# Optimization experiments

Hardware: AMD Instinct MI355X
Metric: run time of the kernel (lower is better)

## Reference

```python
import jax, jax.numpy as jnp
import numpy as np
import math

NUM_HEADS = 16
HEAD_DIM = 64
NUM_BUCKETS = 256
MAX_DISTANCE = 16384
ROPE_BASE = 10000.0


def _rel_pos_bucket(rel):
    # faithful to RelativePositionEncoding._relative_position_bucket
    ab = jnp.abs(rel)
    max_exact = NUM_BUCKETS // 4  # 64
    half = NUM_BUCKETS // 2       # 128
    is_small = ab < max_exact
    safe = jnp.maximum(ab, 1).astype(jnp.float32)
    large = max_exact + (jnp.log(safe / max_exact) / math.log(MAX_DISTANCE / max_exact) * (half - max_exact)).astype(jnp.int32)
    large = jnp.minimum(large, half - 1)
    bucket = jnp.where(is_small, ab, large)
    bucket = jnp.where(rel < 0, half + bucket, bucket)
    return bucket


def _rope_cos_sin(seq_len):
    # RotaryPositionEncoding with rope dim = 2*head_dim: num_features = head_dim,
    # inv_freq over arange(0, head_dim, 2)/head_dim, interleaved repeat to head_dim
    inv_freq = 1.0 / (ROPE_BASE ** (jnp.arange(0, HEAD_DIM, 2, dtype=jnp.float32) / HEAD_DIM))
    pos = jnp.arange(seq_len, dtype=jnp.float32)
    freqs = pos[:, None] * inv_freq[None, :]          # [S, HEAD_DIM//2]
    cos = jnp.repeat(jnp.cos(freqs), 2, axis=-1)      # [S, HEAD_DIM]
    sin = jnp.repeat(jnp.sin(freqs), 2, axis=-1)
    return cos, sin


def _rotate_half(t):
    h = t.shape[-1] // 2
    return jnp.concatenate([-t[..., h:], t[..., :h]], axis=-1)


def setup_inputs() -> dict:
    key = jax.random.key(0)
    ks = jax.random.split(key, 6)
    B, S, E = 2, 2048, 1024
    x = jax.random.normal(ks[0], (B, S, E), dtype=jnp.float32)
    Wq = jax.random.normal(ks[1], (E, E), dtype=jnp.float32) * 0.02
    Wk = jax.random.normal(ks[2], (E, E), dtype=jnp.float32) * 0.02
    Wv = jax.random.normal(ks[3], (E, E), dtype=jnp.float32) * 0.02
    Wo = jax.random.normal(ks[4], (E, E), dtype=jnp.float32) * 0.02
    rel_emb = jax.random.normal(ks[5], (NUM_BUCKETS, NUM_HEADS, HEAD_DIM), dtype=jnp.float32) * 0.02
    return {"x": x, "Wq": Wq, "Wk": Wk, "Wv": Wv, "Wo": Wo, "rel_emb": rel_emb}


def reference(x, Wq, Wk, Wv, Wo, rel_emb):
    B, S, E = x.shape
    H, D = NUM_HEADS, HEAD_DIM

    def split_heads(t):
        return t.reshape(B, S, H, D).transpose(0, 2, 1, 3)  # [B,H,S,D]

    q = split_heads(x @ Wq)
    k = split_heads(x @ Wk)
    v = split_heads(x @ Wv)

    # inline RoPE on q/k (cos/sin broadcast over batch & heads)
    cos, sin = _rope_cos_sin(S)  # [S, D]
    q = q * cos + _rotate_half(q) * sin
    k = k * cos + _rotate_half(k) * sin

    # relative-position bucket bias: q . rel_emb[bucket(i-j)]
    pos = jnp.arange(S)
    bucket = _rel_pos_bucket(pos[:, None] - pos[None, :])      # [S, S]
    q_rel = jnp.einsum('bhqd,nhd->bhqn', q, rel_emb)           # [B,H,S,NUM_BUCKETS]
    bias = jnp.take_along_axis(q_rel, bucket[None, None, :, :], axis=-1)  # [B,H,S,S]

    scale = 1.0 / math.sqrt(D)
    scores = (jnp.einsum('bhqd,bhkd->bhqk', q, k) + bias) * scale

    causal = pos[:, None] >= pos[None, :]
    scores = jnp.where(causal[None, None], scores, jnp.float32(-1e9))
    attn = jax.nn.softmax(scores, axis=-1)

    out = jnp.einsum('bhqk,bhkd->bhqd', attn, v)
    out = out.transpose(0, 2, 1, 3).reshape(B, S, E)
    return out @ Wo
```

## Files before the change

kernel.cpp:

```cpp
#include <hip/hip_runtime.h>
#include <hip/hip_bf16.h>
#include <math.h>


typedef __attribute__((ext_vector_type(8))) short bf16x8;
typedef __attribute__((ext_vector_type(4))) float f32x4;

static __device__ __forceinline__ unsigned short f2bf(float x) {
    unsigned u = __float_as_uint(x);
    unsigned r = (u + 0x7fffu + ((u >> 16) & 1u)) >> 16;
    return (unsigned short)r;
}
static __device__ __forceinline__ float bf2f(unsigned short h) {
    return __uint_as_float(((unsigned)h) << 16);
}
static __device__ __forceinline__ unsigned cvtpk(float lo, float hi) {
    unsigned r;
    asm("v_cvt_pk_bf16_f32 %0, %1, %2" : "=v"(r) : "v"(lo), "v"(hi));
    return r;
}
static __device__ __forceinline__ float fexp2(float x) {
    return __builtin_amdgcn_exp2f(x);
}

#define GLOAD16(gp, lp)                                                            \
    __builtin_amdgcn_global_load_lds(                                              \
        (const __attribute__((address_space(1))) unsigned int*)(gp),               \
        (__attribute__((address_space(3))) unsigned int*)(lp), 16, 0, 0)

__global__ void prep(const float* __restrict__ x,
                     const float* __restrict__ W0, const float* __restrict__ W1,
                     const float* __restrict__ W2, const float* __restrict__ W3,
                     const float* __restrict__ rel,
                     unsigned short* __restrict__ xb,
                     unsigned short* __restrict__ T0, unsigned short* __restrict__ T1,
                     unsigned short* __restrict__ T2, unsigned short* __restrict__ T3,
                     unsigned short* __restrict__ relTb)
{
    __shared__ unsigned short tls[64][65];
    const int id  = blockIdx.x;
    const int tid = threadIdx.x;
    if (id < 2048) {
        const size_t t = (size_t)id * 256 + tid;
        const float4* p = (const float4*)(x + t*8);
        float4 a = p[0], b = p[1];
        unsigned w0 = cvtpk(a.x, a.y), w1 = cvtpk(a.z, a.w);
        unsigned w2 = cvtpk(b.x, b.y), w3 = cvtpk(b.z, b.w);
        *(uint4*)(xb + t*8) = make_uint4(w0, w1, w2, w3);
    } else if (id < 3072) {
        const int local = id - 2048;
        const int z  = local >> 8;
        const float* W = (z == 0) ? W0 : (z == 1) ? W1 : (z == 2) ? W2 : W3;
        unsigned short* Wt = (z == 0) ? T0 : (z == 1) ? T1 : (z == 2) ? T2 : T3;
        const int bb  = local & 255;
        const int bxt = bb & 15;
        const int byt = bb >> 4;
        const int r   = tid >> 2;
        const int c0  = (tid & 3) * 16;
        const float* src = W + (size_t)(byt*64 + r)*1024 + bxt*64 + c0;
#pragma unroll
        for (int j = 0; j < 4; ++j) {
            float4 vv = ((const float4*)src)[j];
            tls[c0 + j*4 + 0][r] = f2bf(vv.x);
            tls[c0 + j*4 + 1][r] = f2bf(vv.y);
            tls[c0 + j*4 + 2][r] = f2bf(vv.z);
            tls[c0 + j*4 + 3][r] = f2bf(vv.w);
        }
        __syncthreads();
        unsigned short* dst = Wt + (size_t)(bxt*64 + r)*1024 + byt*64 + c0;
        unsigned w[8];
#pragma unroll
        for (int j = 0; j < 8; ++j)
            w[j] = (unsigned)tls[r][c0 + 2*j] | ((unsigned)tls[r][c0 + 2*j + 1] << 16);
        *(uint4*)(dst)     = make_uint4(w[0], w[1], w[2], w[3]);
        *(uint4*)(dst + 8) = make_uint4(w[4], w[5], w[6], w[7]);
    } else {
        const int t  = (id - 3072) * 256 + tid;
        const int d0 = (t & 7) * 8;
        const int n  = (t >> 3) & 127;
        const int h  = t >> 10;
        const float* src = rel + ((size_t)(n*16 + h))*64 + d0;
        float4 a = ((const float4*)src)[0], b = ((const float4*)src)[1];
        unsigned w0 = cvtpk(a.x, a.y), w1 = cvtpk(a.z, a.w);
        unsigned w2 = cvtpk(b.x, b.y), w3 = cvtpk(b.z, b.w);
        *(uint4*)(relTb + (size_t)h*8192 + n*64 + d0) = make_uint4(w0, w1, w2, w3);
    }
}

#define GEMM_STAGE(t, buf)                                                             \
    {                                                                                  \
        const int k0s = (t) * 64;                                                      \
        _Pragma("unroll")                                                              \
        for (int j = 0; j < 4; ++j) {                                                  \
            GLOAD16(agp + (size_t)(j*32 + srow)*1024 + k0s, &Als[buf][0] + j*2048 + tid*8); \
            GLOAD16(bgp + (size_t)(j*32 + srow)*1024 + k0s, &Bls[buf][0] + j*2048 + tid*8); \
        }                                                                              \
    }

#define GEMM_COMPUTE(buf)                                                              \
    {                                                                                  \
        _Pragma("unroll")                                                              \
        for (int ks = 0; ks < 2; ++ks) {                                               \
            bf16x8 af[4], bfr[4];                                                      \
            _Pragma("unroll")                                                          \
            for (int m = 0; m < 4; ++m)                                                \
                af[m] = *(const bf16x8*)&Als[buf][(wr + m*16 + (lane & 15))*64 + ks*32 + (lane >> 4)*8]; \
            _Pragma("unroll")                                                          \
            for (int n = 0; n < 4; ++n)                                                \
                bfr[n] = *(const bf16x8*)&Bls[buf][(wc + n*16 + (lane & 15))*64 + ks*32 + (lane >> 4)*8]; \
            _Pragma("unroll")                                                          \
            for (int m = 0; m < 4; ++m)                                                \
                _Pragma("unroll")                                                      \
                for (int n = 0; n < 4; ++n)                                            \
                    acc[m][n] = __builtin_amdgcn_mfma_f32_16x16x32_bf16(af[m], bfr[n], acc[m][n], 0, 0, 0); \
        }                                                                              \
    }

__global__ __launch_bounds__(256) void gemm_qkv(const unsigned short* __restrict__ A,
    const unsigned short* __restrict__ wtq, const unsigned short* __restrict__ wtk,
    const unsigned short* __restrict__ wtv,
    unsigned short* __restrict__ qb, unsigned short* __restrict__ kbb,
    unsigned short* __restrict__ vTb)
{
    __shared__ __align__(16) unsigned short Als[2][8192];
    __shared__ __align__(16) unsigned short Bls[2][8192];
    const int z = blockIdx.z;
    const unsigned short* Bt = (z == 0) ? wtq : (z == 1) ? wtk : wtv;

    const int tid  = threadIdx.x;
    const int wave = tid >> 6, lane = tid & 63;
    const int wr = (wave >> 1) * 64, wc = (wave & 1) * 64;
    const int bx = blockIdx.x, by = blockIdx.y;
    const int srow = tid >> 3;
    const unsigned short* agp = A  + (size_t)(by*128)*1024 + (tid & 7)*8;
    const unsigned short* bgp = Bt + (size_t)(bx*128)*1024 + (tid & 7)*8;

    f32x4 acc[4][4];
#pragma unroll
    for (int m = 0; m < 4; ++m)
#pragma unroll
        for (int n = 0; n < 4; ++n) acc[m][n] = (f32x4)0.f;

    GEMM_STAGE(0, 0);
    __syncthreads();
    int cur = 0;
    for (int t = 0; t < 16; ++t) {
        if (t < 15) GEMM_STAGE(t + 1, cur ^ 1);
        GEMM_COMPUTE(cur);
        __syncthreads();
        cur ^= 1;
    }

    if (z == 2) {
#pragma unroll
        for (int m = 0; m < 4; ++m) {
            const int r0 = by*128 + wr + m*16 + (lane >> 4)*4;
#pragma unroll
            for (int n = 0; n < 4; ++n) {
                const int col = bx*128 + wc + n*16 + (lane & 15);
                const int bb = r0 >> 11, ss = r0 & 2047;
                const int hh = col >> 6, dd = col & 63;
                unsigned r01 = cvtpk(acc[m][n][0], acc[m][n][1]);
                unsigned r23 = cvtpk(acc[m][n][2], acc[m][n][3]);
                *(uint2*)(vTb + (((size_t)bb*16 + hh)*64 + dd)*2048 + ss) = make_uint2(r01, r23);
            }
        }
    } else {
        unsigned short* O = z ? kbb : qb;
        const float CC = 0.41524101186092029f;
        const float qscl = z ? 1.0f : 0.1803368801111204f;
#pragma unroll
        for (int n = 0; n < 2; ++n) {
            const int dd = n*16 + (lane & 15);
            const float if0 = exp2f(-(float)(dd >> 1) * CC);
            const float if1 = exp2f(-(float)(16 + (dd >> 1)) * CC);
            const int col = bx*128 + wc + n*16 + (lane & 15);
            const int hh = col >> 6;
#pragma unroll
            for (int m = 0; m < 4; ++m) {
                const int r0 = by*128 + wr + m*16 + (lane >> 4)*4;
#pragma unroll
                for (int rg = 0; rg < 4; ++rg) {
                    const int row = r0 + rg;
                    const int bb = row >> 11, s = row & 2047;
                    const float x0 = acc[m][n][rg];
                    const float x1 = acc[m][n + 2][rg];
                    const float a0 = (float)s * if0;
                    const float a1 = (float)s * if1;
                    const float o0 = (x0 * __cosf(a0) - x1 * __sinf(a0)) * qscl;
                    const float o1 = (x1 * __cosf(a1) + x0 * __sinf(a1)) * qscl;
                    unsigned short* ob = O + (((size_t)bb*16 + hh)*2048 + s)*64 + dd;
                    ob[0]  = f2bf(o0);
                    ob[32] = f2bf(o1);
                }
            }
        }
    }
}

__global__ __launch_bounds__(256) void gemm_o(const unsigned short* __restrict__ A,
                                              const unsigned short* __restrict__ Bt,
                                              float* __restrict__ C)
{
    __shared__ __align__(16) unsigned short Als[2][8192];
    __shared__ __align__(16) unsigned short Bls[2][8192];
    const int tid  = threadIdx.x;
    const int wave = tid >> 6, lane = tid & 63;
    const int wr = (wave >> 1) * 64, wc = (wave & 1) * 64;
    const int bx = blockIdx.x, by = blockIdx.y;
    const int srow = tid >> 3;
    const unsigned short* agp = A  + (size_t)(by*128)*1024 + (tid & 7)*8;
    const unsigned short* bgp = Bt + (size_t)(bx*128)*1024 + (tid & 7)*8;

    f32x4 acc[4][4];
#pragma unroll
    for (int m = 0; m < 4; ++m)
#pragma unroll
        for (int n = 0; n < 4; ++n) acc[m][n] = (f32x4)0.f;

    GEMM_STAGE(0, 0);
    __syncthreads();
    int cur = 0;
    for (int t = 0; t < 16; ++t) {
        if (t < 15) GEMM_STAGE(t + 1, cur ^ 1);
        GEMM_COMPUTE(cur);
        __syncthreads();
        cur ^= 1;
    }

#pragma unroll
    for (int m = 0; m < 4; ++m) {
        const int r0 = by*128 + wr + m*16 + (lane >> 4)*4;
#pragma unroll
        for (int n = 0; n < 4; ++n) {
            const int col = bx*128 + wc + n*16 + (lane & 15);
#pragma unroll
            for (int rg = 0; rg < 4; ++rg)
                C[(size_t)(r0 + rg)*1024 + col] = acc[m][n][rg];
        }
    }
}

__global__ __launch_bounds__(256) void qrel_mfma(const unsigned short* __restrict__ qb,
                                                 const unsigned short* __restrict__ relTb,
                                                 unsigned short* __restrict__ qrelb)
{
    __shared__ __align__(16) unsigned short Rls[8192];
    __shared__ __align__(16) unsigned short Qls[8192];
    const int tid  = threadIdx.x;
    const int wave = tid >> 6, lane = tid & 63;
    const int wr = (wave >> 1) * 64;
    const int wc = (wave & 1) * 64;
    const int s0 = blockIdx.x * 128;
    const int bh = blockIdx.y;
    const int h  = bh & 15;

    const unsigned short* qsrc = qb + ((size_t)bh*2048 + s0)*64;
    const unsigned short* rsrc = relTb + (size_t)h*8192;
#pragma unroll
    for (int j = 0; j < 4; ++j) {
        GLOAD16(rsrc + j*2048 + tid*8, &Rls[0] + j*2048 + tid*8);
        GLOAD16(qsrc + j*2048 + tid*8, &Qls[0] + j*2048 + tid*8);
    }

    f32x4 acc[4][4];
#pragma unroll
    for (int m = 0; m < 4; ++m)
#pragma unroll
        for (int n = 0; n < 4; ++n) acc[m][n] = (f32x4)0.f;

    __syncthreads();

#pragma unroll
    for (int ks = 0; ks < 2; ++ks) {
        bf16x8 rf[4], qf[4];
#pragma unroll
        for (int m = 0; m < 4; ++m)
            rf[m] = *(const bf16x8*)&Rls[(wr + m*16 + (lane & 15))*64 + ks*32 + (lane >> 4)*8];
#pragma unroll
        for (int n = 0; n < 4; ++n)
            qf[n] = *(const bf16x8*)&Qls[(wc + n*16 + (lane & 15))*64 + ks*32 + (lane >> 4)*8];
#pragma unroll
        for (int m = 0; m < 4; ++m)
#pragma unroll
            for (int n = 0; n < 4; ++n)
                acc[m][n] = __builtin_amdgcn_mfma_f32_16x16x32_bf16(rf[m], qf[n], acc[m][n], 0, 0, 0);
    }

#pragma unroll
    for (int m = 0; m < 4; ++m) {
        const int bkt0 = wr + m*16 + (lane >> 4)*4;
#pragma unroll
        for (int n = 0; n < 4; ++n) {
            const int srow = s0 + wc + n*16 + (lane & 15);
            unsigned r01 = cvtpk(acc[m][n][0], acc[m][n][1]);
            unsigned r23 = cvtpk(acc[m][n][2], acc[m][n][3]);
            *(uint2*)(qrelb + ((size_t)bh*2048 + srow)*128 + bkt0) = make_uint2(r01, r23);
        }
    }
}

__global__ __launch_bounds__(256) void flash_mfma(
    const unsigned short* __restrict__ qb, const unsigned short* __restrict__ kb,
    const unsigned short* __restrict__ vT, const unsigned short* __restrict__ qrelb,
    unsigned short* __restrict__ ctxb)
{
    __shared__ __align__(16) unsigned short kls[2][4096];
    __shared__ __align__(16) unsigned short vtls[2][4096];
    __shared__ __align__(16) unsigned short qrels[64*136];
    __shared__ unsigned short btbl[2048];

    const int tid = threadIdx.x;
    const int id  = blockIdx.x;
    const int bh  = id & 31;
    const int px  = id >> 5;

    const int w   = tid >> 6;
    const int l   = tid & 63;
    const int q15 = l & 15;
    const int g   = l >> 4;

    for (int idx = tid; idx < 2048; idx += 256) {
        int bkt;
        if (idx < 64) bkt = idx;
        else {
            bkt = 64 + (int)(__log2f((float)idx) * 8.0f - 48.0f);
            bkt = bkt > 127 ? 127 : bkt;
        }
        btbl[idx] = (unsigned short)(bkt * 2);
    }

    const size_t headoff = (size_t)bh * 2048 * 64;
    const unsigned short* gbase;
    int jstride;
    if (tid < 128) { gbase = kb + headoff; jstride = 64; }
    else           { gbase = vT + headoff; jstride = 1;  }
    int soff[4], doff[4];
#pragma unroll
    for (int i = 0; i < 4; ++i) {
        const int D = (tid & 127)*16 + i*2048;
        const int r = D >> 7, c = (D >> 4) & 7;
        soff[i] = (tid < 128) ? (r*64 + ((c ^ (r & 7))*8))
                              : (r*2048 + ((c ^ (r & 7))*8));
        doff[i] = D;
    }

    const char* qrow_base = (const char*)qrels + (w*16 + q15) * 272;
    const int srcA = ((2*g) & 3)*16 + q15;
    const int srcB = ((2*g + 1) & 3)*16 + q15;

    int cur = 0;
    for (int pp = 0; pp < 2; ++pp) {
        const int bxc = pp ? (31 - px) : px;
        const int i0  = bxc * 64;
        const int iq  = i0 + w*16 + q15;

        __syncthreads();
        for (int idx = tid; idx < 1024; idx += 256) {
            const int r = idx >> 4, c8 = idx & 15;
            uint4 vv = *(const uint4*)(qrelb + ((size_t)bh*2048 + i0 + r)*128 + c8*8);
            *(uint4*)&qrels[r*136 + c8*8] = vv;
        }
        {
            char* lb = (tid < 128) ? (char*)kls[cur] : (char*)vtls[cur];
#pragma unroll
            for (int i = 0; i < 4; ++i) GLOAD16(gbase + soff[i], lb + doff[i]);
        }

        bf16x8 qf0, qf1;
        {
            const unsigned short* qrow = qb + ((size_t)bh*2048 + i0 + w*16 + q15)*64;
            qf0 = *(const bf16x8*)(qrow + g*8);
            qf1 = *(const bf16x8*)(qrow + 32 + g*8);
        }

        f32x4 acc[4];
#pragma unroll
        for (int d = 0; d < 4; ++d) acc[d] = (f32x4)0.f;
        float mrun = -INFINITY, lsum = 0.f;

        __syncthreads();

        const int ntiles = bxc + 1;
        for (int t = 0; t < ntiles; ++t) {
            const int j0 = t * 64;
            if (t + 1 < ntiles) {
                const unsigned short* gt = gbase + (size_t)(j0 + 64) * jstride;
                char* lb = (tid < 128) ? (char*)kls[cur ^ 1] : (char*)vtls[cur ^ 1];
#pragma unroll
                for (int i = 0; i < 4; ++i) GLOAD16(gt + soff[i], lb + doff[i]);
            }

            f32x4 s[4];
#pragma unroll
            for (int ss = 0; ss < 4; ++ss) s[ss] = (f32x4)0.f;
#pragma unroll
            for (int ks = 0; ks < 2; ++ks) {
                const bf16x8 qq = ks ? qf1 : qf0;
                const int gr = ((ks*4 + g) ^ (q15 & 7)) * 8;
#pragma unroll
                for (int ss = 0; ss < 4; ++ss) {
                    bf16x8 kf = *(const bf16x8*)&kls[cur][(ss*16 + q15)*64 + gr];
                    s[ss] = __builtin_amdgcn_mfma_f32_16x16x32_bf16(kf, qq, s[ss], 0, 0, 0);
                }
            }

            const int relbase = iq - j0 - g*4;
            float sv[16];
            float tmax = -INFINITY;
            if (t != bxc) {
#pragma unroll
                for (int ss = 0; ss < 4; ++ss) {
#pragma unroll
                    for (int r = 0; r < 4; ++r) {
                        const int bi = relbase - ss*16 - r;
                        const float bias = bf2f(*(const unsigned short*)(qrow_base + btbl[bi]));
                        const float val = s[ss][r] + bias;
                        sv[ss*4 + r] = val;
                        tmax = fmaxf(tmax, val);
                    }
                }
            } else {
#pragma unroll
                for (int ss = 0; ss < 4; ++ss) {
#pragma unroll
                    for (int r = 0; r < 4; ++r) {
                        const int rel = relbase - ss*16 - r;
                        const int bi = rel < 0 ? 0 : rel;
                        const float bias = bf2f(*(const unsigned short*)(qrow_base + btbl[bi]));
                        float val = s[ss][r] + bias;
                        val = (rel >= 0) ? val : -1e30f;
                        sv[ss*4 + r] = val;
                        tmax = fmaxf(tmax, val);
                    }
                }
            }
            tmax = fmaxf(tmax, __shfl_xor(tmax, 16));
            tmax = fmaxf(tmax, __shfl_xor(tmax, 32));

            float newm = mrun;
            if (!__all(tmax - mrun <= 8.0f)) {
                newm = fmaxf(mrun, tmax);
                const float corr = fexp2(mrun - newm);
                lsum *= corr;
#pragma unroll
                for (int d = 0; d < 4; ++d) {
                    acc[d][0] *= corr; acc[d][1] *= corr; acc[d][2] *= corr; acc[d][3] *= corr;
                }
                mrun = newm;
            }

            float p[16], ps = 0.f;
#pragma unroll
            for (int j = 0; j < 16; ++j) { p[j] = fexp2(sv[j] - newm); ps += p[j]; }
            ps += __shfl_xor(ps, 16);
            ps += __shfl_xor(ps, 32);
            lsum += ps;

#pragma unroll
            for (int ck = 0; ck < 2; ++ck) {
                unsigned w00 = cvtpk(p[8*ck+0], p[8*ck+1]);
                unsigned w01 = cvtpk(p[8*ck+2], p[8*ck+3]);
                unsigned w10 = cvtpk(p[8*ck+4], p[8*ck+5]);
                unsigned w11 = cvtpk(p[8*ck+6], p[8*ck+7]);
                unsigned a0 = (unsigned)__shfl((int)w00, srcA);
                unsigned b0 = (unsigned)__shfl((int)w10, srcA);
                unsigned a1 = (unsigned)__shfl((int)w01, srcA);
                unsigned b1 = (unsigned)__shfl((int)w11, srcA);
                unsigned a2 = (unsigned)__shfl((int)w00, srcB);
                unsigned b2 = (unsigned)__shfl((int)w10, srcB);
                unsigned a3 = (unsigned)__shfl((int)w01, srcB);
                unsigned b3 = (unsigned)__shfl((int)w11, srcB);
                union { unsigned u[4]; bf16x8 v; } pu;
                pu.u[0] = (g < 2) ? a0 : b0;
                pu.u[1] = (g < 2) ? a1 : b1;
                pu.u[2] = (g < 2) ? a2 : b2;
                pu.u[3] = (g < 2) ? a3 : b3;
#pragma unroll
                for (int dblk = 0; dblk < 4; ++dblk) {
                    const int d2 = dblk*16 + q15;
                    bf16x8 vf = *(const bf16x8*)&vtls[cur][d2*64 + (((ck*4 + g) ^ (d2 & 7))*8)];
                    acc[dblk] = __builtin_amdgcn_mfma_f32_16x16x32_bf16(vf, pu.v, acc[dblk], 0, 0, 0);
                }
            }

            __syncthreads();
            cur ^= 1;
        }

        const float inv = 1.0f / lsum;
        const int s2 = i0 + w*16 + q15;
        const int b2 = bh >> 4, hh = bh & 15;
        unsigned short* obase = ctxb + (((size_t)b2*2048 + s2)*16 + hh)*64;
#pragma unroll
        for (int dblk = 0; dblk < 4; ++dblk) {
            const int d0 = dblk*16 + g*4;
            unsigned r01 = cvtpk(acc[dblk][0]*inv, acc[dblk][1]*inv);
            unsigned r23 = cvtpk(acc[dblk][2]*inv, acc[dblk][3]*inv);
            *(uint2*)(obase + d0) = make_uint2(r01, r23);
        }
    }
}

extern "C" void kernel_launch(void* const* d_in, const int* in_sizes, int n_in,
                              void* d_out, int out_size, void* d_ws, size_t ws_size,
                              hipStream_t stream)
{
    const float* x   = (const float*)d_in[0];
    const float* Wq  = (const float*)d_in[1];
    const float* Wk  = (const float*)d_in[2];
    const float* Wv  = (const float*)d_in[3];
    const float* Wo  = (const float*)d_in[4];
    const float* rel = (const float*)d_in[5];

    float* ws = (float*)d_ws;
    unsigned short* qb    = (unsigned short*)(ws + 8388608);
    unsigned short* kbb   = (unsigned short*)(ws + 10485760);
    unsigned short* qrelb = (unsigned short*)(ws + 12582912);
    unsigned short* vTb   = (unsigned short*)(ws + 16777216);
    unsigned short* xb    = (unsigned short*)(ws + 18874368);
    unsigned short* wtq   = (unsigned short*)(ws + 20971520);
    unsigned short* wtk   = (unsigned short*)(ws + 21495808);
    unsigned short* wtv   = (unsigned short*)(ws + 22020096);
    unsigned short* wto   = (unsigned short*)(ws + 22544384);
    unsigned short* relTb = (unsigned short*)(ws + 23068672);
    unsigned short* ctxb  = (unsigned short*)ws;

    prep<<<3136, 256, 0, stream>>>(x, Wq, Wk, Wv, Wo, rel, xb, wtq, wtk, wtv, wto, relTb);
    gemm_qkv<<<dim3(8, 32, 3), 256, 0, stream>>>(xb, wtq, wtk, wtv, qb, kbb, vTb);
    qrel_mfma<<<dim3(16, 32), 256, 0, stream>>>(qb, relTb, qrelb);
    flash_mfma<<<512, 256, 0, stream>>>(qb, kbb, vTb, qrelb, ctxb);
    gemm_o<<<dim3(8, 32), 256, 0, stream>>>(ctxb, wto, (float*)d_out);
}
```

Baseline: 192.0 us.

## Restructure flash attention into 128-row blocks and precompute RoPE table

The attention kernel now runs 512-thread blocks that each handle one 128-query tile, processed largest-first. This replaces the previous scheme of two 64-row tiles per block paired for causal load balancing, so K/V tiles are shared across eight waves, and waves past their diagonal skip compute. The LDS bucket table is replaced by computing the log bucket inline. RoPE cos/sin values are precomputed once into a table in the prep kernel and read in the QKV GEMM epilogue instead of computing transcendentals there. The risks are idle waves on diagonal tiles, more ALU for inline buckets, and scattered table loads in the epilogue.

```diff
diff --git a/kernel.cpp b/kernel.cpp
--- a/kernel.cpp
+++ b/kernel.cpp
@@ -35,7 +35,7 @@
                      unsigned short* __restrict__ xb,
                      unsigned short* __restrict__ T0, unsigned short* __restrict__ T1,
                      unsigned short* __restrict__ T2, unsigned short* __restrict__ T3,
-                     unsigned short* __restrict__ relTb)
+                     unsigned short* __restrict__ relTb, float* __restrict__ ropeT)
 {
     __shared__ unsigned short tls[64][65];
     const int id  = blockIdx.x;
@@ -74,7 +74,7 @@
             w[j] = (unsigned)tls[r][c0 + 2*j] | ((unsigned)tls[r][c0 + 2*j + 1] << 16);
         *(uint4*)(dst)     = make_uint4(w[0], w[1], w[2], w[3]);
         *(uint4*)(dst + 8) = make_uint4(w[4], w[5], w[6], w[7]);
-    } else {
+    } else if (id < 3136) {
         const int t  = (id - 3072) * 256 + tid;
         const int d0 = (t & 7) * 8;
         const int n  = (t >> 3) & 127;
@@ -84,6 +84,16 @@
         unsigned w0 = cvtpk(a.x, a.y), w1 = cvtpk(a.z, a.w);
         unsigned w2 = cvtpk(b.x, b.y), w3 = cvtpk(b.z, b.w);
         *(uint4*)(relTb + (size_t)h*8192 + n*64 + d0) = make_uint4(w0, w1, w2, w3);
+    } else {
+        const int idx = (id - 3136) * 256 + tid;
+        const int s = idx >> 4, f = idx & 15;
+        const float CC = 0.41524101186092029f;
+        const float if0 = exp2f(-(float)f * CC);
+        const float if1 = exp2f(-(float)(f + 16) * CC);
+        const float a0 = (float)s * if0;
+        const float a1 = (float)s * if1;
+        *(float4*)(ropeT + (size_t)idx*4) =
+            make_float4(__cosf(a0), __sinf(a0), __cosf(a1), __sinf(a1));
     }
 }
 
@@ -118,7 +128,7 @@
 
 __global__ __launch_bounds__(256) void gemm_qkv(const unsigned short* __restrict__ A,
     const unsigned short* __restrict__ wtq, const unsigned short* __restrict__ wtk,
-    const unsigned short* __restrict__ wtv,
+    const unsigned short* __restrict__ wtv, const float* __restrict__ ropeT,
     unsigned short* __restrict__ qb, unsigned short* __restrict__ kbb,
     unsigned short* __restrict__ vTb)
 {
@@ -167,13 +177,11 @@
         }
     } else {
         unsigned short* O = z ? kbb : qb;
-        const float CC = 0.41524101186092029f;
         const float qscl = z ? 1.0f : 0.1803368801111204f;
 #pragma unroll
         for (int n = 0; n < 2; ++n) {
             const int dd = n*16 + (lane & 15);
-            const float if0 = exp2f(-(float)(dd >> 1) * CC);
-            const float if1 = exp2f(-(float)(16 + (dd >> 1)) * CC);
+            const int f  = dd >> 1;
             const int col = bx*128 + wc + n*16 + (lane & 15);
             const int hh = col >> 6;
 #pragma unroll
@@ -183,12 +191,11 @@
                 for (int rg = 0; rg < 4; ++rg) {
                     const int row = r0 + rg;
                     const int bb = row >> 11, s = row & 2047;
+                    const float4 cs = *(const float4*)(ropeT + ((size_t)(s*16 + f))*4);
                     const float x0 = acc[m][n][rg];
                     const float x1 = acc[m][n + 2][rg];
-                    const float a0 = (float)s * if0;
-                    const float a1 = (float)s * if1;
-                    const float o0 = (x0 * __cosf(a0) - x1 * __sinf(a0)) * qscl;
-                    const float o1 = (x1 * __cosf(a1) + x0 * __sinf(a1)) * qscl;
+                    const float o0 = (x0 * cs.x - x1 * cs.y) * qscl;
+                    const float o1 = (x1 * cs.z + x0 * cs.w) * qscl;
                     unsigned short* ob = O + (((size_t)bb*16 + hh)*2048 + s)*64 + dd;
                     ob[0]  = f2bf(o0);
                     ob[32] = f2bf(o1);
@@ -300,97 +307,84 @@
     }
 }
 
-__global__ __launch_bounds__(256) void flash_mfma(
+__global__ __launch_bounds__(512) void flash_mfma(
     const unsigned short* __restrict__ qb, const unsigned short* __restrict__ kb,
     const unsigned short* __restrict__ vT, const unsigned short* __restrict__ qrelb,
     unsigned short* __restrict__ ctxb)
 {
     __shared__ __align__(16) unsigned short kls[2][4096];
     __shared__ __align__(16) unsigned short vtls[2][4096];
-    __shared__ __align__(16) unsigned short qrels[64*136];
-    __shared__ unsigned short btbl[2048];
+    __shared__ __align__(16) unsigned short qrels[128*138];
 
     const int tid = threadIdx.x;
     const int id  = blockIdx.x;
     const int bh  = id & 31;
-    const int px  = id >> 5;
+    const int px  = 15 - (id >> 5);
+    const int i0  = px * 128;
 
     const int w   = tid >> 6;
     const int l   = tid & 63;
     const int q15 = l & 15;
     const int g   = l >> 4;
-
-    for (int idx = tid; idx < 2048; idx += 256) {
-        int bkt;
-        if (idx < 64) bkt = idx;
-        else {
-            bkt = 64 + (int)(__log2f((float)idx) * 8.0f - 48.0f);
-            bkt = bkt > 127 ? 127 : bkt;
-        }
-        btbl[idx] = (unsigned short)(bkt * 2);
-    }
+    const int iq  = i0 + w*16 + q15;
+    const int tdiag  = 2*px + (w >> 2);
+    const int ntiles = 2*px + 2;
 
     const size_t headoff = (size_t)bh * 2048 * 64;
-    const unsigned short* gbase;
-    int jstride;
-    if (tid < 128) { gbase = kb + headoff; jstride = 64; }
-    else           { gbase = vT + headoff; jstride = 1;  }
-    int soff[4], doff[4];
-#pragma unroll
-    for (int i = 0; i < 4; ++i) {
-        const int D = (tid & 127)*16 + i*2048;
+    const int half = tid >> 8;
+    const int t8   = tid & 255;
+    const unsigned short* gbase = half ? (vT + headoff) : (kb + headoff);
+    const int jstride = half ? 1 : 64;
+    int soff[2], doff[2];
+#pragma unroll
+    for (int i = 0; i < 2; ++i) {
+        const int D = t8*16 + i*4096;
         const int r = D >> 7, c = (D >> 4) & 7;
-        soff[i] = (tid < 128) ? (r*64 + ((c ^ (r & 7))*8))
-                              : (r*2048 + ((c ^ (r & 7))*8));
+        soff[i] = half ? (r*2048 + ((c ^ (r & 7))*8)) : (r*64 + ((c ^ (r & 7))*8));
         doff[i] = D;
     }
 
-    const char* qrow_base = (const char*)qrels + (w*16 + q15) * 272;
+    for (int idx = tid; idx < 2048; idx += 512) {
+        const int r = idx >> 4, c8 = idx & 15;
+        uint4 vv = *(const uint4*)(qrelb + ((size_t)bh*2048 + i0 + r)*128 + c8*8);
+        unsigned* d = (unsigned*)&qrels[r*138 + c8*8];
+        d[0] = vv.x; d[1] = vv.y; d[2] = vv.z; d[3] = vv.w;
+    }
+    {
+        char* lb = half ? (char*)vtls[0] : (char*)kls[0];
+#pragma unroll
+        for (int i = 0; i < 2; ++i) GLOAD16(gbase + soff[i], lb + doff[i]);
+    }
+
+    bf16x8 qf0, qf1;
+    {
+        const unsigned short* qrow = qb + ((size_t)bh*2048 + iq)*64;
+        qf0 = *(const bf16x8*)(qrow + g*8);
+        qf1 = *(const bf16x8*)(qrow + 32 + g*8);
+    }
+
+    f32x4 acc[4];
+#pragma unroll
+    for (int d = 0; d < 4; ++d) acc[d] = (f32x4)0.f;
+    float mrun = -INFINITY, lsum = 0.f;
+
+    const int qrow_lds = (w*16 + q15) * 138;
     const int srcA = ((2*g) & 3)*16 + q15;
     const int srcB = ((2*g + 1) & 3)*16 + q15;
 
+    __syncthreads();
+
     int cur = 0;
-    for (int pp = 0; pp < 2; ++pp) {
-        const int bxc = pp ? (31 - px) : px;
-        const int i0  = bxc * 64;
-        const int iq  = i0 + w*16 + q15;
-
-        __syncthreads();
-        for (int idx = tid; idx < 1024; idx += 256) {
-            const int r = idx >> 4, c8 = idx & 15;
-            uint4 vv = *(const uint4*)(qrelb + ((size_t)bh*2048 + i0 + r)*128 + c8*8);
-            *(uint4*)&qrels[r*136 + c8*8] = vv;
-        }
-        {
-            char* lb = (tid < 128) ? (char*)kls[cur] : (char*)vtls[cur];
-#pragma unroll
-            for (int i = 0; i < 4; ++i) GLOAD16(gbase + soff[i], lb + doff[i]);
-        }
-
-        bf16x8 qf0, qf1;
-        {
-            const unsigned short* qrow = qb + ((size_t)bh*2048 + i0 + w*16 + q15)*64;
-            qf0 = *(const bf16x8*)(qrow + g*8);
-            qf1 = *(const bf16x8*)(qrow + 32 + g*8);
-        }
-
-        f32x4 acc[4];
-#pragma unroll
-        for (int d = 0; d < 4; ++d) acc[d] = (f32x4)0.f;
-        float mrun = -INFINITY, lsum = 0.f;
-
-        __syncthreads();
-
-        const int ntiles = bxc + 1;
-        for (int t = 0; t < ntiles; ++t) {
-            const int j0 = t * 64;
-            if (t + 1 < ntiles) {
-                const unsigned short* gt = gbase + (size_t)(j0 + 64) * jstride;
-                char* lb = (tid < 128) ? (char*)kls[cur ^ 1] : (char*)vtls[cur ^ 1];
-#pragma unroll
-                for (int i = 0; i < 4; ++i) GLOAD16(gt + soff[i], lb + doff[i]);
-            }
-
+    for (int t = 0; t < ntiles; ++t) {
+        const int j0 = t * 64;
+        if (t + 1 < ntiles) {
+            const unsigned short* gt = gbase + (size_t)(j0 + 64) * jstride;
+            char* lb = half ? (char*)vtls[cur ^ 1] : (char*)kls[cur ^ 1];
+#pragma unroll
+            for (int i = 0; i < 2; ++i) GLOAD16(gt + soff[i], lb + doff[i]);
+        }
+
+        if (t <= tdiag) {
             f32x4 s[4];
 #pragma unroll
             for (int ss = 0; ss < 4; ++ss) s[ss] = (f32x4)0.f;
@@ -408,13 +402,19 @@
             const int relbase = iq - j0 - g*4;
             float sv[16];
             float tmax = -INFINITY;
-            if (t != bxc) {
+            if (t != tdiag) {
 #pragma unroll
                 for (int ss = 0; ss < 4; ++ss) {
 #pragma unroll
                     for (int r = 0; r < 4; ++r) {
                         const int bi = relbase - ss*16 - r;
-                        const float bias = bf2f(*(const unsigned short*)(qrow_base + btbl[bi]));
+                        int bkt;
+                        if (bi < 64) bkt = bi;
+                        else {
+                            bkt = 64 + (int)(__log2f((float)bi) * 8.0f - 48.0f);
+                            bkt = bkt > 127 ? 127 : bkt;
+                        }
+                        const float bias = bf2f(qrels[qrow_lds + bkt]);
                         const float val = s[ss][r] + bias;
                         sv[ss*4 + r] = val;
                         tmax = fmaxf(tmax, val);
@@ -427,7 +427,13 @@
                     for (int r = 0; r < 4; ++r) {
                         const int rel = relbase - ss*16 - r;
                         const int bi = rel < 0 ? 0 : rel;
-                        const float bias = bf2f(*(const unsigned short*)(qrow_base + btbl[bi]));
+                        int bkt;
+                        if (bi < 64) bkt = bi;
+                        else {
+                            bkt = 64 + (int)(__log2f((float)bi) * 8.0f - 48.0f);
+                            bkt = bkt > 127 ? 127 : bkt;
+                        }
+                        const float bias = bf2f(qrels[qrow_lds + bkt]);
                         float val = s[ss][r] + bias;
                         val = (rel >= 0) ? val : -1e30f;
                         sv[ss*4 + r] = val;
@@ -483,22 +489,22 @@
                     acc[dblk] = __builtin_amdgcn_mfma_f32_16x16x32_bf16(vf, pu.v, acc[dblk], 0, 0, 0);
                 }
             }
-
-            __syncthreads();
-            cur ^= 1;
-        }
-
-        const float inv = 1.0f / lsum;
-        const int s2 = i0 + w*16 + q15;
-        const int b2 = bh >> 4, hh = bh & 15;
-        unsigned short* obase = ctxb + (((size_t)b2*2048 + s2)*16 + hh)*64;
-#pragma unroll
-        for (int dblk = 0; dblk < 4; ++dblk) {
-            const int d0 = dblk*16 + g*4;
-            unsigned r01 = cvtpk(acc[dblk][0]*inv, acc[dblk][1]*inv);
-            unsigned r23 = cvtpk(acc[dblk][2]*inv, acc[dblk][3]*inv);
-            *(uint2*)(obase + d0) = make_uint2(r01, r23);
-        }
+        }
+
+        __syncthreads();
+        cur ^= 1;
+    }
+
+    const float inv = 1.0f / lsum;
+    const int s2 = iq;
+    const int b2 = bh >> 4, hh = bh & 15;
+    unsigned short* obase = ctxb + (((size_t)b2*2048 + s2)*16 + hh)*64;
+#pragma unroll
+    for (int dblk = 0; dblk < 4; ++dblk) {
+        const int d0 = dblk*16 + g*4;
+        unsigned r01 = cvtpk(acc[dblk][0]*inv, acc[dblk][1]*inv);
+        unsigned r23 = cvtpk(acc[dblk][2]*inv, acc[dblk][3]*inv);
+        *(uint2*)(obase + d0) = make_uint2(r01, r23);
     }
 }
 
@@ -524,11 +530,12 @@
     unsigned short* wtv   = (unsigned short*)(ws + 22020096);
     unsigned short* wto   = (unsigned short*)(ws + 22544384);
     unsigned short* relTb = (unsigned short*)(ws + 23068672);
+    float*          ropeT = ws + 23134208;
     unsigned short* ctxb  = (unsigned short*)ws;
 
-    prep<<<3136, 256, 0, stream>>>(x, Wq, Wk, Wv, Wo, rel, xb, wtq, wtk, wtv, wto, relTb);
-    gemm_qkv<<<dim3(8, 32, 3), 256, 0, stream>>>(xb, wtq, wtk, wtv, qb, kbb, vTb);
+    prep<<<3264, 256, 0, stream>>>(x, Wq, Wk, Wv, Wo, rel, xb, wtq, wtk, wtv, wto, relTb, ropeT);
+    gemm_qkv<<<dim3(8, 32, 3), 256, 0, stream>>>(xb, wtq, wtk, wtv, ropeT, qb, kbb, vTb);
     qrel_mfma<<<dim3(16, 32), 256, 0, stream>>>(qb, relTb, qrelb);
-    flash_mfma<<<512, 256, 0, stream>>>(qb, kbb, vTb, qrelb, ctxb);
+    flash_mfma<<<512, 512, 0, stream>>>(qb, kbb, vTb, qrelb, ctxb);
     gemm_o<<<dim3(8, 32), 256, 0, stream>>>(ctxb, wto, (float*)d_out);
 }
```

Result: faster. 185.1 us (-3.6%).
